# Kernel optimization log

Measured on AMD Instinct MI355X. Metric: run time of the kernel, lower is better.

The kernel has to match this reference:

```python
import jax, jax.numpy as jnp
import numpy as np

K_SCOPE = 25.0
K_ENV = 100.0
K_LABEL_4 = 1.5
WIN = int(K_SCOPE) + 2
N = 65536
H = W = 4096


def setup_inputs() -> dict:
    key = jax.random.key(0)
    k1, k2, k3, k4 = jax.random.split(key, 4)
    # positions well inside the map so windows stay (mostly) in bounds
    first_frame = jax.random.uniform(k1, (N, 2), minval=64.0, maxval=H - 64.0)
    current_step = jax.random.normal(k2, (N, 2)) * 5.0
    current_vel = jax.random.normal(k3, (N, 2))
    semantic_map = jax.random.randint(k4, (H, W), 0, 6).astype(jnp.int32)
    F0 = jnp.zeros((N, 2), jnp.float32)
    return {"current_step": current_step, "first_frame": first_frame,
            "current_vel": current_vel, "semantic_map": semantic_map, "F0": F0}


def reference(current_step, first_frame, current_vel, semantic_map, F0):
    Hm, Wm = semantic_map.shape
    ori = current_step + first_frame                      # [N,2]
    scope = ori + jnp.sign(current_vel) * K_SCOPE
    a0 = jnp.floor(ori).astype(jnp.int32)                 # (r0,c0)
    a1 = jnp.floor(scope).astype(jnp.int32)               # (r1,c1)
    r0, c0 = a0[:, 0], a0[:, 1]
    r1, c1 = a1[:, 0], a1[:, 1]
    rmin, rmax = jnp.minimum(r0, r1), jnp.maximum(r0, r1)
    cmin, cmax = jnp.minimum(c0, c1), jnp.maximum(c0, c1)
    deg_r = r0 == r1
    deg_c = c0 == c1

    lr = jnp.arange(WIN)
    lc = jnp.arange(WIN)
    rows = rmin[:, None] + lr[None, :]
    cols = cmin[:, None] + lc[None, :]
    rin = (rows >= 0) & (rows < Hm)
    cin = (cols >= 0) & (cols < Wm)
    # gathered per-agent windows anchored at the region's min corner
    win = semantic_map[jnp.clip(rows, 0, Hm - 1)[:, :, None],
                       jnp.clip(cols, 0, Wm - 1)[:, None, :]]

    # region mask: degenerate axis -> single line at local index 0; else half-open extent
    mr = jnp.where(deg_r[:, None], lr[None, :] == 0, lr[None, :] < (rmax - rmin)[:, None])
    mc = jnp.where(deg_c[:, None], lc[None, :] == 0, lc[None, :] < (cmax - cmin)[:, None])
    both_deg = deg_r & deg_c
    mask = (mr & rin)[:, :, None] & (mc & cin)[:, None, :] & (~both_deg)[:, None, None]

    lr_f = lr.astype(jnp.float32)
    lc_f = lc.astype(jnp.float32)

    def force_for_label(label, weight, plus_one_row):
        match = (mask & (win == label)).astype(jnp.float32)
        cnt = jnp.sum(match, axis=(1, 2))                     # [N]
        denom = jnp.maximum(cnt, 1.0)
        mean_r = jnp.einsum('nrc,r->n', match, lr_f) / denom  # local-coord centroid
        mean_c = jnp.einsum('nrc,c->n', match, lc_f) / denom

        def safe(d):
            return jnp.where(d == 0, 1.0, d)

        # Case A: same row, cols differ (1D horizontal slice)
        disA = jnp.where(c0 < c1, mean_c, K_SCOPE - mean_c)
        dirA = jnp.where((c0 < c1)[:, None], jnp.array([0.0, -1.0]), jnp.array([0.0, 1.0]))
        FA = (weight * K_ENV / safe(disA))[:, None] * dirA
        FA = jnp.where((disA != 0)[:, None], FA, 0.0)

        # Case B: same col, rows differ (1D vertical slice); label-5 quirk adds +1
        disB = jnp.where(r0 < r1, mean_r + plus_one_row, K_SCOPE - mean_r)
        dirB = jnp.where((r0 < r1)[:, None], jnp.array([-1.0, 0.0]), jnp.array([1.0, 0.0]))
        FB = (weight * K_ENV / safe(disB))[:, None] * dirB
        FB = jnp.where((disB != 0)[:, None], FB, 0.0)

        # Case C: full 2D region, force from the corner matching travel direction
        corner = jnp.stack([jnp.where(r0 < r1, 0.0, K_SCOPE),
                            jnp.where(c0 < c1, 0.0, K_SCOPE)], axis=1)   # [N,2]
        obstacle = jnp.stack([mean_r, mean_c], axis=1)
        d = obstacle - corner
        disC = jnp.sqrt(jnp.sum(d * d, axis=1))
        FC = -(weight * K_ENV) * d / (safe(disC) ** 2)[:, None]
        FC = jnp.where((disC != 0)[:, None], FC, 0.0)

        F = jnp.where((deg_r & ~deg_c)[:, None], FA,
                      jnp.where((~deg_r & deg_c)[:, None], FB, FC))
        active = (cnt > 0) & (~both_deg)
        return jnp.where(active[:, None], F, 0.0)

    F2 = jnp.zeros_like(F0)
    F2 = F2 + force_for_label(5, 1.0, 1.0)        # label 5: +1 row-distance quirk
    F2 = F2 + force_for_label(3, 1.0, 0.0)        # label 3
    F2 = F2 + force_for_label(4, K_LABEL_4, 0.0)  # label 4, scaled by k_label_4
    return F2
```

## Files before the change

### kernel.cpp

```cpp
#include <hip/hip_runtime.h>
#include <math.h>

#define HM 4096
#define WM 4096
#define TGRID 32
#define NTILES (TGRID*TGRID)
#define CAP 80
#define POISON 0xAAAAAAAAu
#define SLOTS (NTILES*CAP)
#define SBLOCKS (SLOTS/8)
#define OBLOCKS 64


#define BYTESUM(x) ((int)(((x) * 0x01010101u) >> 24))
#define KSUM(W) ((int)(((W) >> 8) & 0xFFu) + 2 * (int)(((W) >> 16) & 0xFFu) + 3 * (int)((W) >> 24))

struct AgentGeom {
    int r0, c0, r1, c1;
    int rmin, cmin;
    int nr, nc;
    bool deg_r, deg_c, both;
};

__device__ __forceinline__ AgentGeom agent_geom(const float* __restrict__ cstep,
                                                const float* __restrict__ fframe,
                                                const float* __restrict__ cvel, int n)
{
    AgentGeom g;
    const float ori_r = cstep[2*n+0] + fframe[2*n+0];
    const float ori_c = cstep[2*n+1] + fframe[2*n+1];
    const float vr = cvel[2*n+0], vc = cvel[2*n+1];
    const float sgr = (vr > 0.f) ? 1.f : ((vr < 0.f) ? -1.f : 0.f);
    const float sgc = (vc > 0.f) ? 1.f : ((vc < 0.f) ? -1.f : 0.f);
    g.r0 = (int)floorf(ori_r);
    g.c0 = (int)floorf(ori_c);
    g.r1 = (int)floorf(ori_r + sgr * 25.0f);
    g.c1 = (int)floorf(ori_c + sgc * 25.0f);
    g.rmin = min(g.r0, g.r1);
    g.cmin = min(g.c0, g.c1);
    g.deg_r = (g.r0 == g.r1);
    g.deg_c = (g.c0 == g.c1);
    g.both  = g.deg_r && g.deg_c;
    g.nr = g.deg_r ? 1 : min(max(g.r0, g.r1) - g.rmin, 27);
    g.nc = g.deg_c ? 1 : min(max(g.c0, g.c1) - g.cmin, 27);
    return g;
}

__device__ __forceinline__ void force_from_counts(const AgentGeom& g,
    const int cnts[3], const int srs[3], const int scs[3], float& Fr, float& Fc)
{
    const float wts[3] = {1.0f, 1.0f, 1.5f};
    const float p1s[3] = {1.0f, 0.0f, 0.0f};
    Fr = 0.0f; Fc = 0.0f;
    #pragma unroll
    for (int i = 0; i < 3; ++i) {
        const float denom  = fmaxf((float)cnts[i], 1.0f);
        const float mean_r = (float)srs[i] / denom;
        const float mean_c = (float)scs[i] / denom;
        float fr, fc;
        if (g.deg_r && !g.deg_c) {
            const float disA = (g.c0 < g.c1) ? mean_c : (25.0f - mean_c);
            const float mag  = (disA != 0.0f) ? (wts[i] * 100.0f / disA) : 0.0f;
            fr = 0.0f;
            fc = (g.c0 < g.c1) ? -mag : mag;
        } else if (!g.deg_r && g.deg_c) {
            const float disB = (g.r0 < g.r1) ? (mean_r + p1s[i]) : (25.0f - mean_r);
            const float mag  = (disB != 0.0f) ? (wts[i] * 100.0f / disB) : 0.0f;
            fr = (g.r0 < g.r1) ? -mag : mag;
            fc = 0.0f;
        } else {
            const float crn_r = (g.r0 < g.r1) ? 0.0f : 25.0f;
            const float crn_c = (g.c0 < g.c1) ? 0.0f : 25.0f;
            const float dr = mean_r - crn_r;
            const float dc = mean_c - crn_c;
            const float disC = sqrtf(dr * dr + dc * dc);
            if (disC != 0.0f) {
                const float s = -(wts[i] * 100.0f) / (disC * disC);
                fr = s * dr; fc = s * dc;
            } else { fr = 0.0f; fc = 0.0f; }
        }
        if (cnts[i] > 0 && !g.both) { Fr += fr; Fc += fc; }
    }
}

__device__ __forceinline__ int agent_tile(const float* __restrict__ cstep,
                                          const float* __restrict__ fframe, int n)
{
    const float orr = cstep[2*n+0] + fframe[2*n+0];
    const float occ = cstep[2*n+1] + fframe[2*n+1];
    const int r = min(max((int)floorf(orr), 0), HM - 1);
    const int c = min(max((int)floorf(occ), 0), WM - 1);
    return ((r >> 7) << 5) | (c >> 7);
}

__global__ __launch_bounds__(256) void nsp_place(
    const float* __restrict__ cstep, const float* __restrict__ fframe,
    unsigned* __restrict__ wsw, int N)
{
    const int n = blockIdx.x * blockDim.x + threadIdx.x;
    if (n >= N) return;
    unsigned* tcnt  = wsw;
    unsigned* ocnt  = wsw + NTILES;
    int*      olist = (int*)(ocnt + 1);
    int*      slot  = olist + N;
    const int t = agent_tile(cstep, fframe, n);
    const unsigned rank = atomicAdd(&tcnt[t], 1u) - POISON;
    if (rank < CAP) {
        slot[t * CAP + rank] = n;
    } else {
        const unsigned op = atomicAdd(ocnt, 1u) - POISON;
        olist[op] = n;
    }
}

__device__ __forceinline__ void gather_body_int(
    const float* __restrict__ cstep, const float* __restrict__ fframe,
    const float* __restrict__ cvel, const int* __restrict__ smap,
    float* __restrict__ out, int n, bool live, int lane)
{
    const int l5  = lane & 31;
    const AgentGeom g = agent_geom(cstep, fframe, cvel, n);

    const int cg  = l5 & 7;
    const int rho = l5 >> 3;
    const int a   = g.cmin & ~3;
    const int d   = g.cmin - a;

    unsigned B = 0;
    #pragma unroll
    for (int k = 0; k < 4; ++k) {
        const int wc  = cg * 4 + k - d;
        const int col = a + cg * 4 + k;
        const bool bad = ((unsigned)wc >= (unsigned)g.nc) ||
                         ((unsigned)col >= (unsigned)WM);
        B |= bad ? (0xFFu << (8 * k)) : 0u;
    }

    const int T_half = (g.nr + 3) >> 2;
    const int t_lane = (rho < g.nr) ? ((g.nr - rho + 3) >> 2) : 0;
    const int T_oth  = __shfl_xor(T_half, 32);
    const int T_wave = max(T_half, T_oth);

    const bool fastl = (g.rmin >= 0) && (g.rmin + 28 <= HM) &&
                       (a >= 0) && (a + 32 <= WM);
    const bool fastw = __all(fastl ? 1 : 0);

    unsigned W5 = 0, S5 = 0, W3 = 0, S3 = 0, W4 = 0, S4 = 0;
    const unsigned k01 = 0x01010101u;

    if (fastw) {
        const int* p = smap + (size_t)(g.rmin + rho) * WM + a + cg * 4;
        #pragma unroll 2
        for (int j = 0; j < T_wave; ++j) {
            const int4 v = *reinterpret_cast<const int4*>(p);
            p += 4 * WM;
            unsigned y = ((((((unsigned)v.w << 8) | (unsigned)v.z) << 8)
                           | (unsigned)v.y) << 8) | (unsigned)v.x;
            y |= B;
            y = (j < t_lane) ? y : 0xFFFFFFFFu;
            const unsigned b1 = y >> 1, b2 = y >> 2;
            const unsigned m5 = ( y & ~b1 &  b2) & k01;
            const unsigned m3 = ( y &  b1 & ~b2) & k01;
            const unsigned m4 = (~y & ~b1 &  b2) & k01;
            W5 += m5; S5 += W5;
            W3 += m3; S3 += W3;
            W4 += m4; S4 += W4;
        }
    } else {
        for (int j = 0; j < T_wave; ++j) {
            const int rrow = g.rmin + rho + 4 * j;
            const int rcl  = min(max(rrow, 0), HM - 1);
            unsigned y = 0;
            #pragma unroll
            for (int k = 0; k < 4; ++k) {
                const int col  = a + cg * 4 + k;
                const int colc = min(max(col, 0), WM - 1);
                y |= ((unsigned)smap[(size_t)rcl * WM + colc]) << (8 * k);
            }
            y |= B;
            const bool rok = (j < t_lane) && ((unsigned)rrow < (unsigned)HM);
            y = rok ? y : 0xFFFFFFFFu;
            const unsigned b1 = y >> 1, b2 = y >> 2;
            const unsigned m5 = ( y & ~b1 &  b2) & k01;
            const unsigned m3 = ( y &  b1 & ~b2) & k01;
            const unsigned m4 = (~y & ~b1 &  b2) & k01;
            W5 += m5; S5 += W5;
            W3 += m3; S3 += W3;
            W4 += m4; S4 += W4;
        }
    }

    const int c5 = BYTESUM(W5), c3 = BYTESUM(W3), c4 = BYTESUM(W4);
    const int rs5 = rho * c5 + 4 * (T_wave * c5 - BYTESUM(S5));
    const int rs3 = rho * c3 + 4 * (T_wave * c3 - BYTESUM(S3));
    const int rs4 = rho * c4 + 4 * (T_wave * c4 - BYTESUM(S4));
    const int cbase = cg * 4 - d;
    const int cs5  = cbase * c5 + KSUM(W5);
    const int cs3  = cbase * c3 + KSUM(W3);
    const int cs4v = cbase * c4 + KSUM(W4);

    unsigned q5 = (unsigned)c5 | ((unsigned)rs5 << 10);
    unsigned q3 = (unsigned)c3 | ((unsigned)rs3 << 10);
    unsigned q4 = (unsigned)c4 | ((unsigned)rs4 << 10);
    unsigned scp = (unsigned)cs5 | ((unsigned)cs3 << 15);
    int      sc4 = cs4v;

    #pragma unroll
    for (int o = 1; o <= 16; o <<= 1) {
        q5  += __shfl_xor(q5, o);
        q3  += __shfl_xor(q3, o);
        q4  += __shfl_xor(q4, o);
        scp += __shfl_xor(scp, o);
        sc4 += __shfl_xor(sc4, o);
    }

    if (l5 == 0 && live) {
        const int cnts[3] = {(int)(q5 & 1023u), (int)(q3 & 1023u), (int)(q4 & 1023u)};
        const int srs[3]  = {(int)(q5 >> 10),   (int)(q3 >> 10),   (int)(q4 >> 10)};
        const int scs[3]  = {(int)(scp & 0x7FFFu), (int)(scp >> 15), sc4};
        float Fr, Fc;
        force_from_counts(g, cnts, srs, scs, Fr, Fc);
        out[2*n+0] = Fr;
        out[2*n+1] = Fc;
    }
}

__global__ __launch_bounds__(256) void nsp_gather_s(
    const float* __restrict__ cstep, const float* __restrict__ fframe,
    const float* __restrict__ cvel, const int* __restrict__ smap,
    const unsigned* __restrict__ wsw, float* __restrict__ out, int N)
{
    const unsigned* tcnt  = wsw;
    const unsigned* ocnt  = wsw + NTILES;
    const int*      olist = (const int*)(ocnt + 1);
    const int*      slot  = olist + N;

    const int lane = threadIdx.x & 63;
    const int half = lane >> 5;
    const int widx = threadIdx.x >> 6;

    if (blockIdx.x < SBLOCKS) {
        const int cpx = SBLOCKS >> 3;
        const int bid = ((int)blockIdx.x & 7) * cpx + ((int)blockIdx.x >> 3);
        const int sid = bid * 8 + widx * 2 + half;
        const int t   = sid / CAP;
        const int s   = sid - t * CAP;
        const unsigned cnt = min(tcnt[t] - POISON, (unsigned)CAP);
        const bool live = (unsigned)s < cnt;
        if (__ballot(live ? 1 : 0) == 0ull) return;
        const int n = live ? slot[t * CAP + s] : 0;
        gather_body_int(cstep, fframe, cvel, smap, out, n, live, lane);
    } else {
        const int ow  = ((int)blockIdx.x - SBLOCKS) * 4 + widx;
        const int OW  = OBLOCKS * 4;
        unsigned oc = ocnt[0] - POISON;
        if (oc > (unsigned)N) oc = 0;
        for (int base = ow * 2; base < (int)oc; base += OW * 2) {
            const int i = base + half;
            const bool live = i < (int)oc;
            const int n = live ? olist[i] : 0;
            gather_body_int(cstep, fframe, cvel, smap, out, n, live, lane);
        }
    }
}

__global__ __launch_bounds__(256) void nsp_gather_flat(
    const float* __restrict__ cstep, const float* __restrict__ fframe,
    const float* __restrict__ cvel, const int* __restrict__ smap,
    float* __restrict__ out, int N)
{
    const int wave = (blockIdx.x * blockDim.x + threadIdx.x) >> 6;
    const int lane = threadIdx.x & 63;
    const int half = lane >> 5;
    const int n    = wave * 2 + half;
    const bool live = (n < N);
    const int n_eff = live ? n : (N - 1);
    gather_body_int(cstep, fframe, cvel, smap, out, n_eff, live, lane);
}

extern "C" void kernel_launch(void* const* d_in, const int* in_sizes, int n_in,
                              void* d_out, int out_size, void* d_ws, size_t ws_size,
                              hipStream_t stream) {
    const float* cstep  = (const float*)d_in[0];
    const float* fframe = (const float*)d_in[1];
    const float* cvel   = (const float*)d_in[2];
    const int*   smap   = (const int*)d_in[3];
    float* out = (float*)d_out;

    const int N = in_sizes[0] / 2;
    const size_t need = (size_t)(NTILES + 1 + N + SLOTS) * sizeof(int);

    if (d_ws != nullptr && ws_size >= need) {
        unsigned* wsw = (unsigned*)d_ws;
        hipLaunchKernelGGL(nsp_place, dim3((N + 255) / 256), dim3(256), 0, stream,
                           cstep, fframe, wsw, N);
        hipLaunchKernelGGL(nsp_gather_s, dim3(SBLOCKS + OBLOCKS), dim3(256), 0, stream,
                           cstep, fframe, cvel, smap, wsw, out, N);
    } else {
        const int waves  = (N + 1) / 2;
        const int blocks = (waves * 64 + 255) / 256;
        hipLaunchKernelGGL(nsp_gather_flat, dim3(blocks), dim3(256), 0, stream,
                           cstep, fframe, cvel, smap, out, N);
    }
}
```

Baseline: 142.9 us.

## Fuse place and gather via cooperative grid sync, pack four agents per wave

Merges the tile-binning kernel and the gather kernel into one cooperative kernel that bins agents, syncs the whole grid, then processes virtual blocks in a grid-stride loop. Each wave now handles four agents with 16 lanes each (two row phases instead of four), which halves lane waste on the 27-wide windows and shortens the shuffle reduction. Byte packing uses v_perm, and a safer byte sum is used because per-byte prefix sums can now exceed 255. The costs are the grid-wide barrier and host-side device-property and occupancy queries on every launch, plus longer per-lane loops.

```diff
diff --git a/kernel.cpp b/kernel.cpp
--- a/kernel.cpp
+++ b/kernel.cpp
@@ -1,4 +1,5 @@
 #include <hip/hip_runtime.h>
+#include <hip/hip_cooperative_groups.h>
 #include <math.h>
 
 #define HM 4096
@@ -8,12 +9,16 @@
 #define CAP 80
 #define POISON 0xAAAAAAAAu
 #define SLOTS (NTILES*CAP)
-#define SBLOCKS (SLOTS/8)
+#define VBLOCKS (SLOTS/16)
 #define OBLOCKS 64
 
 
 #define BYTESUM(x) ((int)(((x) * 0x01010101u) >> 24))
 #define KSUM(W) ((int)(((W) >> 8) & 0xFFu) + 2 * (int)(((W) >> 16) & 0xFFu) + 3 * (int)((W) >> 24))
+__device__ __forceinline__ int bytesum_safe(unsigned x) {
+    unsigned t = (x & 0x00FF00FFu) + ((x >> 8) & 0x00FF00FFu);
+    return (int)((t + (t >> 16)) & 0xFFFFu);
+}
 
 struct AgentGeom {
     int r0, c0, r1, c1;
@@ -93,36 +98,16 @@
     return ((r >> 7) << 5) | (c >> 7);
 }
 
-__global__ __launch_bounds__(256) void nsp_place(
-    const float* __restrict__ cstep, const float* __restrict__ fframe,
-    unsigned* __restrict__ wsw, int N)
-{
-    const int n = blockIdx.x * blockDim.x + threadIdx.x;
-    if (n >= N) return;
-    unsigned* tcnt  = wsw;
-    unsigned* ocnt  = wsw + NTILES;
-    int*      olist = (int*)(ocnt + 1);
-    int*      slot  = olist + N;
-    const int t = agent_tile(cstep, fframe, n);
-    const unsigned rank = atomicAdd(&tcnt[t], 1u) - POISON;
-    if (rank < CAP) {
-        slot[t * CAP + rank] = n;
-    } else {
-        const unsigned op = atomicAdd(ocnt, 1u) - POISON;
-        olist[op] = n;
-    }
-}
-
-__device__ __forceinline__ void gather_body_int(
+__device__ __forceinline__ void gather_body4(
     const float* __restrict__ cstep, const float* __restrict__ fframe,
     const float* __restrict__ cvel, const int* __restrict__ smap,
     float* __restrict__ out, int n, bool live, int lane)
 {
-    const int l5  = lane & 31;
+    const int l4  = lane & 15;
     const AgentGeom g = agent_geom(cstep, fframe, cvel, n);
 
-    const int cg  = l5 & 7;
-    const int rho = l5 >> 3;
+    const int cg  = l4 & 7;
+    const int rho = l4 >> 3;
     const int a   = g.cmin & ~3;
     const int d   = g.cmin - a;
 
@@ -136,10 +121,10 @@
         B |= bad ? (0xFFu << (8 * k)) : 0u;
     }
 
-    const int T_half = (g.nr + 3) >> 2;
-    const int t_lane = (rho < g.nr) ? ((g.nr - rho + 3) >> 2) : 0;
-    const int T_oth  = __shfl_xor(T_half, 32);
-    const int T_wave = max(T_half, T_oth);
+    const int T      = (g.nr + 1) >> 1;
+    const int t_lane = (rho < g.nr) ? ((g.nr - rho + 1) >> 1) : 0;
+    int Tw = max(T, __shfl_xor(T, 16));
+    Tw = max(Tw, __shfl_xor(Tw, 32));
 
     const bool fastl = (g.rmin >= 0) && (g.rmin + 28 <= HM) &&
                        (a >= 0) && (a + 32 <= WM);
@@ -151,11 +136,11 @@
     if (fastw) {
         const int* p = smap + (size_t)(g.rmin + rho) * WM + a + cg * 4;
         #pragma unroll 2
-        for (int j = 0; j < T_wave; ++j) {
+        for (int j = 0; j < Tw; ++j) {
             const int4 v = *reinterpret_cast<const int4*>(p);
-            p += 4 * WM;
-            unsigned y = ((((((unsigned)v.w << 8) | (unsigned)v.z) << 8)
-                           | (unsigned)v.y) << 8) | (unsigned)v.x;
+            p += 2 * WM;
+            unsigned y = __builtin_amdgcn_perm((unsigned)v.y, (unsigned)v.x, 0x0C0C0400u)
+                       | __builtin_amdgcn_perm((unsigned)v.w, (unsigned)v.z, 0x04000C0Cu);
             y |= B;
             y = (j < t_lane) ? y : 0xFFFFFFFFu;
             const unsigned b1 = y >> 1, b2 = y >> 2;
@@ -167,8 +152,8 @@
             W4 += m4; S4 += W4;
         }
     } else {
-        for (int j = 0; j < T_wave; ++j) {
-            const int rrow = g.rmin + rho + 4 * j;
+        for (int j = 0; j < Tw; ++j) {
+            const int rrow = g.rmin + rho + 2 * j;
             const int rcl  = min(max(rrow, 0), HM - 1);
             unsigned y = 0;
             #pragma unroll
@@ -191,9 +176,9 @@
     }
 
     const int c5 = BYTESUM(W5), c3 = BYTESUM(W3), c4 = BYTESUM(W4);
-    const int rs5 = rho * c5 + 4 * (T_wave * c5 - BYTESUM(S5));
-    const int rs3 = rho * c3 + 4 * (T_wave * c3 - BYTESUM(S3));
-    const int rs4 = rho * c4 + 4 * (T_wave * c4 - BYTESUM(S4));
+    const int rs5 = rho * c5 + 2 * (Tw * c5 - bytesum_safe(S5));
+    const int rs3 = rho * c3 + 2 * (Tw * c3 - bytesum_safe(S3));
+    const int rs4 = rho * c4 + 2 * (Tw * c4 - bytesum_safe(S4));
     const int cbase = cg * 4 - d;
     const int cs5  = cbase * c5 + KSUM(W5);
     const int cs3  = cbase * c3 + KSUM(W3);
@@ -206,7 +191,7 @@
     int      sc4 = cs4v;
 
     #pragma unroll
-    for (int o = 1; o <= 16; o <<= 1) {
+    for (int o = 1; o <= 8; o <<= 1) {
         q5  += __shfl_xor(q5, o);
         q3  += __shfl_xor(q3, o);
         q4  += __shfl_xor(q4, o);
@@ -214,7 +199,7 @@
         sc4 += __shfl_xor(sc4, o);
     }
 
-    if (l5 == 0 && live) {
+    if (l4 == 0 && live) {
         const int cnts[3] = {(int)(q5 & 1023u), (int)(q3 & 1023u), (int)(q4 & 1023u)};
         const int srs[3]  = {(int)(q5 >> 10),   (int)(q3 >> 10),   (int)(q4 >> 10)};
         const int scs[3]  = {(int)(scp & 0x7FFFu), (int)(scp >> 15), sc4};
@@ -225,41 +210,56 @@
     }
 }
 
-__global__ __launch_bounds__(256) void nsp_gather_s(
+__global__ __launch_bounds__(256, 8) void nsp_fused(
     const float* __restrict__ cstep, const float* __restrict__ fframe,
     const float* __restrict__ cvel, const int* __restrict__ smap,
-    const unsigned* __restrict__ wsw, float* __restrict__ out, int N)
-{
-    const unsigned* tcnt  = wsw;
-    const unsigned* ocnt  = wsw + NTILES;
-    const int*      olist = (const int*)(ocnt + 1);
-    const int*      slot  = olist + N;
+    unsigned* __restrict__ wsw, float* __restrict__ out, int N)
+{
+    unsigned* tcnt  = wsw;
+    unsigned* ocnt  = wsw + NTILES;
+    int*      olist = (int*)(ocnt + 1);
+    int*      slot  = olist + N;
+
+    const int gsize = gridDim.x * blockDim.x;
+    for (int n = blockIdx.x * blockDim.x + threadIdx.x; n < N; n += gsize) {
+        const int t = agent_tile(cstep, fframe, n);
+        const unsigned rank = atomicAdd(&tcnt[t], 1u) - POISON;
+        if (rank < CAP) {
+            slot[t * CAP + rank] = n;
+        } else {
+            const unsigned op = atomicAdd(ocnt, 1u) - POISON;
+            olist[op] = n;
+        }
+    }
+
+    __threadfence();
+    cooperative_groups::this_grid().sync();
 
     const int lane = threadIdx.x & 63;
-    const int half = lane >> 5;
+    const int sub  = lane >> 4;
     const int widx = threadIdx.x >> 6;
 
-    if (blockIdx.x < SBLOCKS) {
-        const int cpx = SBLOCKS >> 3;
-        const int bid = ((int)blockIdx.x & 7) * cpx + ((int)blockIdx.x >> 3);
-        const int sid = bid * 8 + widx * 2 + half;
-        const int t   = sid / CAP;
-        const int s   = sid - t * CAP;
-        const unsigned cnt = min(tcnt[t] - POISON, (unsigned)CAP);
-        const bool live = (unsigned)s < cnt;
-        if (__ballot(live ? 1 : 0) == 0ull) return;
-        const int n = live ? slot[t * CAP + s] : 0;
-        gather_body_int(cstep, fframe, cvel, smap, out, n, live, lane);
-    } else {
-        const int ow  = ((int)blockIdx.x - SBLOCKS) * 4 + widx;
-        const int OW  = OBLOCKS * 4;
-        unsigned oc = ocnt[0] - POISON;
-        if (oc > (unsigned)N) oc = 0;
-        for (int base = ow * 2; base < (int)oc; base += OW * 2) {
-            const int i = base + half;
-            const bool live = i < (int)oc;
-            const int n = live ? olist[i] : 0;
-            gather_body_int(cstep, fframe, cvel, smap, out, n, live, lane);
+    for (int vb = blockIdx.x; vb < VBLOCKS + OBLOCKS; vb += gridDim.x) {
+        if (vb < VBLOCKS) {
+            const int bid = (vb & 7) * (VBLOCKS >> 3) + (vb >> 3);
+            const int sid = bid * 16 + widx * 4 + sub;
+            const int t   = sid / CAP;
+            const int s   = sid - t * CAP;
+            const unsigned cnt = min(tcnt[t] - POISON, (unsigned)CAP);
+            const bool live = (unsigned)s < cnt;
+            if (__ballot(live ? 1 : 0) == 0ull) continue;
+            const int n = live ? slot[t * CAP + s] : 0;
+            gather_body4(cstep, fframe, cvel, smap, out, n, live, lane);
+        } else {
+            const int ow = vb - VBLOCKS;
+            unsigned oc = ocnt[0] - POISON;
+            if (oc > (unsigned)N) oc = 0;
+            for (int base = ow * 16 + widx * 4; base < (int)oc; base += OBLOCKS * 16) {
+                const int i = base + sub;
+                const bool live = i < (int)oc;
+                const int n = live ? olist[i] : 0;
+                gather_body4(cstep, fframe, cvel, smap, out, n, live, lane);
+            }
         }
     }
 }
@@ -271,11 +271,10 @@
 {
     const int wave = (blockIdx.x * blockDim.x + threadIdx.x) >> 6;
     const int lane = threadIdx.x & 63;
-    const int half = lane >> 5;
-    const int n    = wave * 2 + half;
-    const bool live = (n < N);
-    const int n_eff = live ? n : (N - 1);
-    gather_body_int(cstep, fframe, cvel, smap, out, n_eff, live, lane);
+    const int sub  = lane >> 4;
+    const int idx  = wave * 4 + sub;
+    const bool live = (idx < N);
+    gather_body4(cstep, fframe, cvel, smap, out, live ? idx : 0, live, lane);
 }
 
 extern "C" void kernel_launch(void* const* d_in, const int* in_sizes, int n_in,
@@ -292,13 +291,27 @@
 
     if (d_ws != nullptr && ws_size >= need) {
         unsigned* wsw = (unsigned*)d_ws;
-        hipLaunchKernelGGL(nsp_place, dim3((N + 255) / 256), dim3(256), 0, stream,
-                           cstep, fframe, wsw, N);
-        hipLaunchKernelGGL(nsp_gather_s, dim3(SBLOCKS + OBLOCKS), dim3(256), 0, stream,
-                           cstep, fframe, cvel, smap, wsw, out, N);
+
+        int dev = 0;
+        hipGetDevice(&dev);
+        int cus = 256;
+        hipDeviceProp_t prop;
+        if (hipGetDeviceProperties(&prop, dev) == hipSuccess && prop.multiProcessorCount > 0)
+            cus = prop.multiProcessorCount;
+        int maxB = 0;
+        if (hipOccupancyMaxActiveBlocksPerMultiprocessor(&maxB, nsp_fused, 256, 0) != hipSuccess || maxB < 1)
+            maxB = 1;
+        int grid = maxB * cus;
+        if (grid > 2048) grid = 2048;
+
+        const float* a0 = cstep; const float* a1 = fframe; const float* a2 = cvel;
+        const int* a3 = smap; unsigned* a4 = wsw; float* a5 = out; int a6 = N;
+        void* args[] = {&a0, &a1, &a2, &a3, &a4, &a5, &a6};
+        hipLaunchCooperativeKernel((const void*)nsp_fused, dim3(grid), dim3(256),
+                                   args, 0, stream);
     } else {
-        const int waves  = (N + 1) / 2;
-        const int blocks = (waves * 64 + 255) / 256;
+        const int waves  = (N + 3) / 4;
+        const int blocks = (waves + 3) / 4;
         hipLaunchKernelGGL(nsp_gather_flat, dim3(blocks), dim3(256), 0, stream,
                            cstep, fframe, cvel, smap, out, N);
     }
```

After: 287.3 us. 2.01x slower.
